# Kernel tuning notes

Measured on AMD Instinct MI355X. Metric: run time of the kernel, lower is better.

Reference implementation:

```python
import jax, jax.numpy as jnp
import numpy as np

SQ = 1.0 / np.sqrt(2.0)

def _haar_filters():
    dec_lo = np.array([SQ, SQ], np.float32); dec_hi = np.array([-SQ, SQ], np.float32)
    rec_lo = np.array([SQ, SQ], np.float32); rec_hi = np.array([SQ, -SQ], np.float32)
    def bank(lo, hi):
        ks = []
        for fz in (lo, hi):
            for fy in (lo, hi):
                for fx in (lo, hi):
                    ks.append(np.einsum('i,j,k->ijk', fz, fy, fx))
        return jnp.asarray(np.stack(ks, 0))  # [8,2,2,2]
    return bank(dec_lo, dec_hi), bank(rec_lo, rec_hi)

WT_F, IWT_F = _haar_filters()

def dwt3(x):
    # stride-2 2x2x2 cross-correlation == reshape + einsum (kernel size == stride)
    B, C, D, H, W = x.shape
    xr = x.reshape(B, C, D // 2, 2, H // 2, 2, W // 2, 2)
    return jnp.einsum('bcdzhywx,fzyx->bcfdhw', xr, WT_F)  # [B,C,8,D/2,H/2,W/2]

def idwt3(x):
    # conv_transpose3d stride 2 kernel 2: no overlap -> einsum + reshape
    B, C, _, D, H, W = x.shape
    out = jnp.einsum('bcfdhw,fzyx->bcdzhywx', x, IWT_F)
    return out.reshape(B, C, 2 * D, 2 * H, 2 * W)

def dwconv3(x, w, b=None):
    # depthwise 3x3x3 conv, padding SAME (torch padding='same', groups=C)
    y = jax.lax.conv_general_dilated(
        x, w, (1, 1, 1), 'SAME',
        dimension_numbers=('NCDHW', 'OIDHW', 'NCDHW'),
        feature_group_count=x.shape[1])
    if b is not None:
        y = y + b[None, :, None, None, None]
    return y

WT_LEVELS = 2

def setup_inputs() -> dict:
    key = jax.random.key(0)
    ks = jax.random.split(key, 6)
    B, C, D, H, W = 1, 64, 64, 64, 64
    return {
        'x': jax.random.normal(ks[0], (B, C, D, H, W), jnp.float32),
        'base_w': jax.random.normal(ks[1], (C, 1, 3, 3, 3), jnp.float32) * 0.1,
        'base_b': jax.random.normal(ks[2], (C,), jnp.float32) * 0.02,
        'base_scale_w': jnp.ones((1, C, 1, 1, 1), jnp.float32),
        'wconv_w0': jax.random.normal(ks[3], (C * 8, 1, 3, 3, 3), jnp.float32) * 0.1,
        'wconv_w1': jax.random.normal(ks[4], (C * 8, 1, 3, 3, 3), jnp.float32) * 0.1,
        'wscale0': jnp.full((1, C * 8, 1, 1, 1), 0.1, jnp.float32),
        'wscale1': jnp.full((1, C * 8, 1, 1, 1), 0.1, jnp.float32),
        'lambd': jnp.float32(0.05),
    }

def reference(x, base_w, base_b, base_scale_w, wconv_w0, wconv_w1, wscale0, wscale1, lambd):
    wconv_ws = (wconv_w0, wconv_w1)
    wscales = (wscale0, wscale1)
    lls, hfs, shapes = [], [], []
    cur = x
    for i in range(WT_LEVELS):
        shapes.append(cur.shape)
        pd, ph, pw = cur.shape[2] % 2, cur.shape[3] % 2, cur.shape[4] % 2
        if pd or ph or pw:
            cur = jnp.pad(cur, ((0, 0), (0, 0), (0, pd), (0, ph), (0, pw)))
        cx = dwt3(cur)                     # [B,C,8,d,h,w]
        cur = cx[:, :, 0]                  # LL passes to next level
        B, C, _, d, h, w = cx.shape
        t = dwconv3(cx.reshape(B, C * 8, d, h, w), wconv_ws[i])
        t = t.reshape(B, C, 8, d, h, w)
        ll, hf = t[:, :, :1], t[:, :, 1:]
        hf = jnp.sign(hf) * jax.nn.relu(jnp.abs(hf) - lambd)  # soft threshold
        t = jnp.concatenate([ll, hf], axis=2)
        t = (t.reshape(B, C * 8, d, h, w) * wscales[i]).reshape(B, C, 8, d, h, w)
        lls.append(t[:, :, 0]); hfs.append(t[:, :, 1:])
    nxt = jnp.float32(0.0)
    for i in range(WT_LEVELS - 1, -1, -1):
        cll = lls[i] + nxt
        cx = jnp.concatenate([cll[:, :, None], hfs[i]], axis=2)
        nxt = idwt3(cx)
        sh = shapes[i]
        nxt = nxt[:, :, :sh[2], :sh[3], :sh[4]]
    base = dwconv3(x, base_w, base_b) * base_scale_w
    return base + nxt
```

## Files before the change

### kernel.cpp

```cpp
#include <hip/hip_runtime.h>

#define SQ3F 0.35355339059327379f

__device__ __forceinline__ void haar_fwd(const float v[8], float o[8]) {
    float ax[8];
#pragma unroll
    for (int i = 0; i < 4; ++i) {
        float a = v[2 * i], b = v[2 * i + 1];
        ax[2 * i]     = a + b;
        ax[2 * i + 1] = b - a;
    }
    float ay[8];
#pragma unroll
    for (int z = 0; z < 2; ++z)
#pragma unroll
        for (int bx = 0; bx < 2; ++bx) {
            float a = ax[z * 4 + bx], b = ax[z * 4 + 2 + bx];
            ay[z * 4 + bx]     = a + b;
            ay[z * 4 + 2 + bx] = b - a;
        }
#pragma unroll
    for (int j = 0; j < 4; ++j) {
        float a = ay[j], b = ay[4 + j];
        o[j]     = (a + b) * SQ3F;
        o[4 + j] = (b - a) * SQ3F;
    }
}

__device__ __forceinline__ void haar_inv(const float t[8], float o[8]) {
    float az[8];
#pragma unroll
    for (int j = 0; j < 4; ++j) {
        float lo = t[j], hi = t[4 + j];
        az[j]     = lo + hi;
        az[4 + j] = lo - hi;
    }
    float ay[8];
#pragma unroll
    for (int z = 0; z < 2; ++z)
#pragma unroll
        for (int bx = 0; bx < 2; ++bx) {
            float lo = az[z * 4 + bx], hi = az[z * 4 + 2 + bx];
            ay[z * 4 + bx]     = lo + hi;
            ay[z * 4 + 2 + bx] = lo - hi;
        }
#pragma unroll
    for (int i = 0; i < 4; ++i) {
        float lo = ay[2 * i], hi = ay[2 * i + 1];
        o[2 * i]     = (lo + hi) * SQ3F;
        o[2 * i + 1] = (lo - hi) * SQ3F;
    }
}

__global__ __launch_bounds__(512, 4) void fused_l0_k(
    const float* __restrict__ x, const float* __restrict__ wt,
    const float* __restrict__ wscale, const float* __restrict__ lambd_p,
    float* __restrict__ t0, float* __restrict__ ll) {
    __shared__ float pl[8][32][35];
    int bx   = blockIdx.x;
    int slab = bx & 7;
    int c    = bx >> 3;
    int z0   = slab * 4;
    int tid  = threadIdx.x;

    {
        int fi   = tid >> 6;
        int rowi = (tid >> 1) & 31;
        pl[fi][rowi][(tid & 1) * 33] = 0.f;
    }

    int f    = __builtin_amdgcn_readfirstlane(tid >> 6);
    int lane = tid & 63;
    int cty  = lane >> 1;
    int cx0i = (lane & 1) * 16;
    int cc   = c * 8 + f;
    float wv[27];
    const float* wp = wt + cc * 27;
#pragma unroll
    for (int k = 0; k < 27; ++k) wv[k] = wp[k];
    float lam = *lambd_p;
    float sc  = wscale[cc];

    const float* xc = x + ((long)c << 18);

    float acc[3][16];
#pragma unroll
    for (int s = 0; s < 3; ++s)
#pragma unroll
        for (int j = 0; j < 16; ++j) acc[s][j] = 0.f;

#pragma unroll
    for (int pp = 0; pp < 6; ++pp) {
        int p       = z0 - 1 + pp;
        bool pvalid = (p >= 0) && (p <= 31);
        __syncthreads();
        if (pvalid) {
#pragma unroll
            for (int half = 0; half < 2; ++half) {
                int cell = tid + half * 512;
                int y = cell >> 5, xx = cell & 31;
                float v[8];
#pragma unroll
                for (int z = 0; z < 2; ++z)
#pragma unroll
                    for (int yy = 0; yy < 2; ++yy) {
                        float2 q = *(const float2*)(xc + (((2 * p + z) << 6) +
                                                          (2 * y + yy)) * 64 + 2 * xx);
                        v[z * 4 + yy * 2]     = q.x;
                        v[z * 4 + yy * 2 + 1] = q.y;
                    }
                float o[8];
                haar_fwd(v, o);
#pragma unroll
                for (int k = 0; k < 8; ++k) pl[k][y][xx + 1] = o[k];
                if (pp >= 1 && pp <= 4)
                    ll[(c << 15) + (p << 10) + cell] = o[0];
            }
        }
        __syncthreads();
        if (pvalid) {
#pragma unroll
            for (int dy = 0; dy < 3; ++dy) {
                int yy = cty - 1 + dy;
                if ((unsigned)yy < 32u) {
                    float r[18];
#pragma unroll
                    for (int k = 0; k < 18; ++k) r[k] = pl[f][yy][cx0i + k];
#pragma unroll
                    for (int dz = 0; dz < 3; ++dz) {
                        constexpr int unused = 0; (void)unused;
                        int rel = pp - dz;
                        if (rel >= 0 && rel <= 3) {
                            int s = rel % 3;
#pragma unroll
                            for (int dx = 0; dx < 3; ++dx) {
                                float wgt = wv[dz * 9 + dy * 3 + dx];
#pragma unroll
                                for (int j = 0; j < 16; ++j)
                                    acc[s][j] += r[dx + j] * wgt;
                            }
                        }
                    }
                }
            }
        }
        {
            int rel = pp - 2;
            if (rel >= 0 && rel <= 3) {
                int zc = z0 + rel;
                int s = rel % 3;
                float res[16];
#pragma unroll
                for (int j = 0; j < 16; ++j) {
                    float t = acc[s][j];
                    if (f != 0) {
                        float a = fabsf(t) - lam;
                        t       = a > 0.f ? copysignf(a, t) : 0.f;
                    }
                    res[j]    = t * sc;
                    acc[s][j] = 0.f;
                }
                float* op = t0 + ((long)cc << 15) + (zc << 10) + cty * 32 + cx0i;
#pragma unroll
                for (int q = 0; q < 4; ++q)
                    *(float4*)(op + q * 4) = float4{res[q * 4], res[q * 4 + 1],
                                                    res[q * 4 + 2], res[q * 4 + 3]};
            }
        }
    }
}

template <int SO>
__global__ __launch_bounds__(256) void dwt3_k(const float* __restrict__ in,
                                              int inChStride,
                                              float* __restrict__ out) {
    constexpr int SI = SO * 2;
    int idx = blockIdx.x * 256 + threadIdx.x;
    int w = idx % SO;
    int h = (idx / SO) % SO;
    int d = (idx / (SO * SO)) % SO;
    int c = idx / (SO * SO * SO);
    const float* ip = in + (long)c * inChStride;
    float v[8];
#pragma unroll
    for (int z = 0; z < 2; ++z)
#pragma unroll
        for (int y = 0; y < 2; ++y) {
            const float2 p =
                *(const float2*)(ip + ((2 * d + z) * SI + (2 * h + y)) * SI + 2 * w);
            v[z * 4 + y * 2]     = p.x;
            v[z * 4 + y * 2 + 1] = p.y;
        }
    float o[8];
    haar_fwd(v, o);
    int s = (d * SO + h) * SO + w;
#pragma unroll
    for (int f = 0; f < 8; ++f) out[(c * 8 + f) * (SO * SO * SO) + s] = o[f];
}

template <int S, int PH>
__device__ __forceinline__ void conv_step(const float* __restrict__ ip, int zo,
                                          int ty, int x0,
                                          const float* __restrict__ wv,
                                          float win[3][3][6], float lam, float sc,
                                          bool hf, float* __restrict__ op) {
    constexpr int sPrev = (PH + 2) % 3;
    constexpr int sCur  = PH;
    constexpr int sNext = (PH + 1) % 3;
    {
        int zz = zo + 1;
        bool zok = zz < S;
        const float* pp = ip + zz * S * S;
#pragma unroll
        for (int dy = 0; dy < 3; ++dy) {
            int yy  = ty - 1 + dy;
            bool yok = zok && ((unsigned)yy < (unsigned)S);
            const float* rp = pp + yy * S;
            win[sNext][dy][0] = (yok && x0 > 0) ? rp[x0 - 1] : 0.f;
            float4 m = yok ? *(const float4*)(rp + x0) : float4{0.f, 0.f, 0.f, 0.f};
            win[sNext][dy][1] = m.x;
            win[sNext][dy][2] = m.y;
            win[sNext][dy][3] = m.z;
            win[sNext][dy][4] = m.w;
            win[sNext][dy][5] = (yok && (x0 + 4 < S)) ? rp[x0 + 4] : 0.f;
        }
    }
    float acc[4] = {0.f, 0.f, 0.f, 0.f};
#pragma unroll
    for (int dz = 0; dz < 3; ++dz) {
        const float(*wp)[6] = (dz == 0) ? win[sPrev] : (dz == 1) ? win[sCur] : win[sNext];
#pragma unroll
        for (int dy = 0; dy < 3; ++dy)
#pragma unroll
            for (int dx = 0; dx < 3; ++dx) {
                float wgt = wv[dz * 9 + dy * 3 + dx];
#pragma unroll
                for (int j = 0; j < 4; ++j) acc[j] += wp[dy][dx + j] * wgt;
            }
    }
    float4 r;
    float* rr = (float*)&r;
#pragma unroll
    for (int j = 0; j < 4; ++j) {
        float t = acc[j];
        if (hf) {
            float a = fabsf(t) - lam;
            t       = a > 0.f ? copysignf(a, t) : 0.f;
        }
        rr[j] = t * sc;
    }
    *(float4*)(op + (zo * S + ty) * S + x0) = r;
}

template <int S, int CPB>
__global__ __launch_bounds__(256) void dwconv_soft_roll_k(
    const float* __restrict__ in, const float* __restrict__ wt,
    const float* __restrict__ wscale, const float* __restrict__ lambd_p,
    float* __restrict__ out) {
    constexpr int TX = S / 4;
    int tid = threadIdx.x;
    int tx  = tid % TX;
    int ty  = (tid / TX) % S;
    int cs  = tid / (TX * S);
    int cc  = blockIdx.x * CPB + cs;
    const float* ip = in + (long)cc * (S * S * S);
    float* op       = out + (long)cc * (S * S * S);
    float wv[27];
#pragma unroll
    for (int k = 0; k < 27; ++k) wv[k] = wt[cc * 27 + k];
    float lam = *lambd_p;
    float sc  = wscale[cc];
    bool hf   = (cc & 7) != 0;
    int x0    = 4 * tx;

    float win[3][3][6];
#pragma unroll
    for (int a = 0; a < 3; ++a)
#pragma unroll
        for (int b = 0; b < 3; ++b)
#pragma unroll
            for (int k = 0; k < 6; ++k) win[a][b][k] = 0.f;
    {
#pragma unroll
        for (int dy = 0; dy < 3; ++dy) {
            int yy  = ty - 1 + dy;
            bool yok = (unsigned)yy < (unsigned)S;
            const float* rp = ip + yy * S;
            win[0][dy][0] = (yok && x0 > 0) ? rp[x0 - 1] : 0.f;
            float4 m = yok ? *(const float4*)(rp + x0) : float4{0.f, 0.f, 0.f, 0.f};
            win[0][dy][1] = m.x;
            win[0][dy][2] = m.y;
            win[0][dy][3] = m.z;
            win[0][dy][4] = m.w;
            win[0][dy][5] = (yok && (x0 + 4 < S)) ? rp[x0 + 4] : 0.f;
        }
    }
#pragma unroll 1
    for (int zb = 0; zb < S; zb += 3) {
        conv_step<S, 0>(ip, zb, ty, x0, wv, win, lam, sc, hf, op);
        if (zb + 1 < S) conv_step<S, 1>(ip, zb + 1, ty, x0, wv, win, lam, sc, hf, op);
        if (zb + 2 < S) conv_step<S, 2>(ip, zb + 2, ty, x0, wv, win, lam, sc, hf, op);
    }
}

__global__ __launch_bounds__(256, 3) void final_k2(
    const float* __restrict__ x, const float* __restrict__ t0,
    const float* __restrict__ t1, const float* __restrict__ bw,
    const float* __restrict__ bb, const float* __restrict__ bscale,
    float* __restrict__ out) {
    __shared__ float xs[18 * 10 * 67];
    int bx = blockIdx.x;
    int c  = bx >> 5;
    int ti = bx & 31;
    int dt = ti >> 3;
    int ht = ti & 7;
    const float* xc = x + ((long)c << 18);
    int zg0 = 16 * dt - 1, yg0 = 8 * ht - 1;
    for (int i = threadIdx.x; i < 18 * 10 * 66; i += 256) {
        int pz = i / 660;
        int r  = i - pz * 660;
        int py = r / 66;
        int px = r - py * 66;
        int zg = zg0 + pz, yg = yg0 + py, xg = px - 1;
        bool ok = ((unsigned)zg < 64u) && ((unsigned)yg < 64u) && ((unsigned)xg < 64u);
        xs[(pz * 10 + py) * 67 + px] = ok ? xc[(zg << 12) + (yg << 6) + xg] : 0.f;
    }
    const float* wp0 = bw + c * 27;
    float wv[27];
#pragma unroll
    for (int k = 0; k < 27; ++k) wv[k] = wp0[k];
    float bias = bb[c], scl = bscale[c];
    __syncthreads();

    int tid = threadIdx.x;
    int wc  = tid & 7;
    int hc  = (tid >> 3) & 3;
    int dc  = tid >> 5;
    int d   = dt * 8 + dc;
    int h   = ht * 4 + hc;
    int w0  = wc * 4;

    float acc[2][2][8];
#pragma unroll
    for (int oz = 0; oz < 2; ++oz)
#pragma unroll
        for (int oy = 0; oy < 2; ++oy)
#pragma unroll
            for (int m = 0; m < 8; ++m) acc[oz][oy][m] = 0.f;

#pragma unroll
    for (int pz = 0; pz < 4; ++pz) {
        float r[4][10];
#pragma unroll
        for (int py = 0; py < 4; ++py)
#pragma unroll
            for (int k = 0; k < 10; ++k)
                r[py][k] = xs[((2 * dc + pz) * 10 + (2 * hc + py)) * 67 + 8 * wc + k];
#pragma unroll
        for (int oz = 0; oz < 2; ++oz) {
            int kz = pz - oz;
            if (kz >= 0 && kz <= 2) {
#pragma unroll
                for (int py = 0; py < 4; ++py)
#pragma unroll
                    for (int oy = 0; oy < 2; ++oy) {
                        int ky = py - oy;
                        if (ky >= 0 && ky <= 2) {
#pragma unroll
                            for (int kx = 0; kx < 3; ++kx) {
                                float wgt = wv[kz * 9 + ky * 3 + kx];
#pragma unroll
                                for (int m = 0; m < 8; ++m)
                                    acc[oz][oy][m] += r[py][m + kx] * wgt;
                            }
                        }
                    }
            }
        }
    }

    int cell0 = (d << 10) + (h << 5) + w0;
    float4 t0v[8];
#pragma unroll
    for (int f = 0; f < 8; ++f)
        t0v[f] = *(const float4*)(t0 + (((long)(c * 8 + f)) << 15) + cell0);
    int s1b = ((d >> 1) * 16 + (h >> 1)) * 16 + (w0 >> 1);
    float2 t1v[8];
#pragma unroll
    for (int f = 0; f < 8; ++f)
        t1v[f] = *(const float2*)(t1 + ((c * 8 + f) << 12) + s1b);

#pragma unroll
    for (int j = 0; j < 4; ++j) {
        int w = w0 + j;
        float tf[8];
#pragma unroll
        for (int f = 0; f < 8; ++f) tf[f] = ((const float*)&t0v[f])[j];
        float add = 0.f;
#pragma unroll
        for (int f = 0; f < 8; ++f) {
            float v  = (j >> 1) ? t1v[f].y : t1v[f].x;
            float sg = 1.f;
            if ((f & 4) && (d & 1)) sg = -sg;
            if ((f & 2) && (h & 1)) sg = -sg;
            if ((f & 1) && (j & 1)) sg = -sg;
            add += sg * v;
        }
        tf[0] += add * SQ3F;
        float contrib[8];
        haar_inv(tf, contrib);
#pragma unroll
        for (int oz = 0; oz < 2; ++oz)
#pragma unroll
            for (int oy = 0; oy < 2; ++oy) {
                float2 rr;
                rr.x = (acc[oz][oy][2 * j] + bias) * scl + contrib[oz * 4 + oy * 2];
                rr.y = (acc[oz][oy][2 * j + 1] + bias) * scl +
                       contrib[oz * 4 + oy * 2 + 1];
                *(float2*)(out + ((long)c << 18) + ((2 * d + oz) << 12) +
                           ((2 * h + oy) << 6) + 2 * w) = rr;
            }
    }
}

extern "C" void kernel_launch(void* const* d_in, const int* in_sizes, int n_in,
                              void* d_out, int out_size, void* d_ws, size_t ws_size,
                              hipStream_t stream) {
    const float* x      = (const float*)d_in[0];
    const float* base_w = (const float*)d_in[1];
    const float* base_b = (const float*)d_in[2];
    const float* base_s = (const float*)d_in[3];
    const float* w0     = (const float*)d_in[4];
    const float* w1     = (const float*)d_in[5];
    const float* ws0    = (const float*)d_in[6];
    const float* ws1    = (const float*)d_in[7];
    const float* lambd  = (const float*)d_in[8];
    float* out = (float*)d_out;

    float* ll  = (float*)d_ws;
    float* t0  = ll + 2097152;
    float* cx1 = t0 + 16777216;
    float* t1  = cx1 + 2097152;

    fused_l0_k<<<512, 512, 0, stream>>>(x, w0, ws0, lambd, t0, ll);
    dwt3_k<16><<<1024, 256, 0, stream>>>(ll, 32768, cx1);
    dwconv_soft_roll_k<16, 4><<<128, 256, 0, stream>>>(cx1, w1, ws1, lambd, t1);
    final_k2<<<2048, 256, 0, stream>>>(x, t0, t1, base_w, base_b, base_s, out);
}
```

Before: 251.6 us.

## Shrink final kernel tiles to one x-cell pair per thread with vector LDS and stores

Halves the depth tile of the final base-conv plus inverse-Haar kernel, so each thread computes 4 output x positions instead of 8. The grid doubles and launch bounds allow 6 blocks per CU. The shared tile pitch becomes 68 so rows can be read with float4/float2 LDS loads, and outputs are written as float4. This trades more halo reloads and more blocks for higher occupancy, fewer registers and wider memory accesses.

```diff
diff --git a/kernel.cpp b/kernel.cpp
--- a/kernel.cpp
+++ b/kernel.cpp
@@ -303,27 +303,27 @@
     }
 }
 
-__global__ __launch_bounds__(256, 3) void final_k2(
+__global__ __launch_bounds__(256, 6) void final_k3(
     const float* __restrict__ x, const float* __restrict__ t0,
     const float* __restrict__ t1, const float* __restrict__ bw,
     const float* __restrict__ bb, const float* __restrict__ bscale,
     float* __restrict__ out) {
-    __shared__ float xs[18 * 10 * 67];
+    __shared__ float xs[10 * 10 * 68];
     int bx = blockIdx.x;
-    int c  = bx >> 5;
-    int ti = bx & 31;
+    int c  = bx >> 6;
+    int ti = bx & 63;
     int dt = ti >> 3;
     int ht = ti & 7;
     const float* xc = x + ((long)c << 18);
-    int zg0 = 16 * dt - 1, yg0 = 8 * ht - 1;
-    for (int i = threadIdx.x; i < 18 * 10 * 66; i += 256) {
+    int zg0 = 8 * dt - 1, yg0 = 8 * ht - 1;
+    for (int i = threadIdx.x; i < 10 * 10 * 66; i += 256) {
         int pz = i / 660;
         int r  = i - pz * 660;
         int py = r / 66;
         int px = r - py * 66;
         int zg = zg0 + pz, yg = yg0 + py, xg = px - 1;
         bool ok = ((unsigned)zg < 64u) && ((unsigned)yg < 64u) && ((unsigned)xg < 64u);
-        xs[(pz * 10 + py) * 67 + px] = ok ? xc[(zg << 12) + (yg << 6) + xg] : 0.f;
+        xs[(pz * 10 + py) * 68 + px] = ok ? xc[(zg << 12) + (yg << 6) + xg] : 0.f;
     }
     const float* wp0 = bw + c * 27;
     float wv[27];
@@ -333,29 +333,33 @@
     __syncthreads();
 
     int tid = threadIdx.x;
-    int wc  = tid & 7;
-    int hc  = (tid >> 3) & 3;
-    int dc  = tid >> 5;
-    int d   = dt * 8 + dc;
+    int wc  = tid & 15;
+    int hc  = (tid >> 4) & 3;
+    int dc  = tid >> 6;
+    int d   = dt * 4 + dc;
     int h   = ht * 4 + hc;
-    int w0  = wc * 4;
-
-    float acc[2][2][8];
+    int x0  = wc * 4;
+
+    float acc[2][2][4];
 #pragma unroll
     for (int oz = 0; oz < 2; ++oz)
 #pragma unroll
         for (int oy = 0; oy < 2; ++oy)
 #pragma unroll
-            for (int m = 0; m < 8; ++m) acc[oz][oy][m] = 0.f;
+            for (int m = 0; m < 4; ++m) acc[oz][oy][m] = 0.f;
 
 #pragma unroll
     for (int pz = 0; pz < 4; ++pz) {
-        float r[4][10];
-#pragma unroll
-        for (int py = 0; py < 4; ++py)
-#pragma unroll
-            for (int k = 0; k < 10; ++k)
-                r[py][k] = xs[((2 * dc + pz) * 10 + (2 * hc + py)) * 67 + 8 * wc + k];
+        float r[4][6];
+#pragma unroll
+        for (int py = 0; py < 4; ++py) {
+            const float* rowp =
+                &xs[((2 * dc + pz) * 10 + (2 * hc + py)) * 68 + x0];
+            float4 a = *(const float4*)rowp;
+            float2 b = *(const float2*)(rowp + 4);
+            r[py][0] = a.x; r[py][1] = a.y; r[py][2] = a.z; r[py][3] = a.w;
+            r[py][4] = b.x; r[py][5] = b.y;
+        }
 #pragma unroll
         for (int oz = 0; oz < 2; ++oz) {
             int kz = pz - oz;
@@ -370,7 +374,7 @@
                             for (int kx = 0; kx < 3; ++kx) {
                                 float wgt = wv[kz * 9 + ky * 3 + kx];
 #pragma unroll
-                                for (int m = 0; m < 8; ++m)
+                                for (int m = 0; m < 4; ++m)
                                     acc[oz][oy][m] += r[py][m + kx] * wgt;
                             }
                         }
@@ -379,48 +383,48 @@
         }
     }
 
-    int cell0 = (d << 10) + (h << 5) + w0;
-    float4 t0v[8];
+    int cell0 = (d << 10) + (h << 5) + 2 * wc;
+    float2 t0v[8];
 #pragma unroll
     for (int f = 0; f < 8; ++f)
-        t0v[f] = *(const float4*)(t0 + (((long)(c * 8 + f)) << 15) + cell0);
-    int s1b = ((d >> 1) * 16 + (h >> 1)) * 16 + (w0 >> 1);
-    float2 t1v[8];
+        t0v[f] = *(const float2*)(t0 + (((long)(c * 8 + f)) << 15) + cell0);
+    int s1b = ((d >> 1) * 16 + (h >> 1)) * 16 + wc;
+    float t1v[8];
 #pragma unroll
     for (int f = 0; f < 8; ++f)
-        t1v[f] = *(const float2*)(t1 + ((c * 8 + f) << 12) + s1b);
-
-#pragma unroll
-    for (int j = 0; j < 4; ++j) {
-        int w = w0 + j;
+        t1v[f] = t1[((c * 8 + f) << 12) + s1b];
+
+    float c0[8], c1[8];
+#pragma unroll
+    for (int j = 0; j < 2; ++j) {
         float tf[8];
 #pragma unroll
-        for (int f = 0; f < 8; ++f) tf[f] = ((const float*)&t0v[f])[j];
+        for (int f = 0; f < 8; ++f) tf[f] = j ? t0v[f].y : t0v[f].x;
         float add = 0.f;
 #pragma unroll
         for (int f = 0; f < 8; ++f) {
-            float v  = (j >> 1) ? t1v[f].y : t1v[f].x;
             float sg = 1.f;
             if ((f & 4) && (d & 1)) sg = -sg;
             if ((f & 2) && (h & 1)) sg = -sg;
-            if ((f & 1) && (j & 1)) sg = -sg;
-            add += sg * v;
+            if ((f & 1) && j) sg = -sg;
+            add += sg * t1v[f];
         }
         tf[0] += add * SQ3F;
-        float contrib[8];
-        haar_inv(tf, contrib);
-#pragma unroll
-        for (int oz = 0; oz < 2; ++oz)
-#pragma unroll
-            for (int oy = 0; oy < 2; ++oy) {
-                float2 rr;
-                rr.x = (acc[oz][oy][2 * j] + bias) * scl + contrib[oz * 4 + oy * 2];
-                rr.y = (acc[oz][oy][2 * j + 1] + bias) * scl +
-                       contrib[oz * 4 + oy * 2 + 1];
-                *(float2*)(out + ((long)c << 18) + ((2 * d + oz) << 12) +
-                           ((2 * h + oy) << 6) + 2 * w) = rr;
-            }
-    }
+        haar_inv(tf, j ? c1 : c0);
+    }
+
+#pragma unroll
+    for (int oz = 0; oz < 2; ++oz)
+#pragma unroll
+        for (int oy = 0; oy < 2; ++oy) {
+            float4 rv;
+            rv.x = (acc[oz][oy][0] + bias) * scl + c0[oz * 4 + oy * 2];
+            rv.y = (acc[oz][oy][1] + bias) * scl + c0[oz * 4 + oy * 2 + 1];
+            rv.z = (acc[oz][oy][2] + bias) * scl + c1[oz * 4 + oy * 2];
+            rv.w = (acc[oz][oy][3] + bias) * scl + c1[oz * 4 + oy * 2 + 1];
+            *(float4*)(out + ((long)c << 18) + ((2 * d + oz) << 12) +
+                       ((2 * h + oy) << 6) + x0) = rv;
+        }
 }
 
 extern "C" void kernel_launch(void* const* d_in, const int* in_sizes, int n_in,
@@ -445,5 +449,5 @@
     fused_l0_k<<<512, 512, 0, stream>>>(x, w0, ws0, lambd, t0, ll);
     dwt3_k<16><<<1024, 256, 0, stream>>>(ll, 32768, cx1);
     dwconv_soft_roll_k<16, 4><<<128, 256, 0, stream>>>(cx1, w1, ws1, lambd, t1);
-    final_k2<<<2048, 256, 0, stream>>>(x, t0, t1, base_w, base_b, base_s, out);
-}
+    final_k3<<<4096, 256, 0, stream>>>(x, t0, t1, base_w, base_b, base_s, out);
+}
```

New measurement: 290.9 us. 1.16x slower.
